# Kernel optimization log

Hardware: AMD Instinct MI355X
Metric: run time of the kernel (lower is better)

The kernel has to match this reference:

```python
import jax, jax.numpy as jnp
import numpy as np

H = 96          # hidden_dim / GatedGraphConv out_channels
L = 6           # num_layers
F_IN = 32       # num_node_features
G = 4096        # number of graphs in batch
BN_EPS = 1e-5


def setup_inputs() -> dict:
    key = jax.random.key(0)
    ks = jax.random.split(key, 16)
    N, E = 100000, 400000
    x = jax.random.normal(ks[0], (N, F_IN), dtype=jnp.float32)
    edge_index = jax.random.randint(ks[1], (2, E), 0, N, dtype=jnp.int64)
    batch = jnp.sort(jax.random.randint(ks[2], (N,), 0, G, dtype=jnp.int64))
    s = 1.0 / np.sqrt(H)
    conv_w = jax.random.uniform(ks[3], (L, H, H), jnp.float32, -s, s)
    w_ih = jax.random.uniform(ks[4], (3 * H, H), jnp.float32, -s, s)
    w_hh = jax.random.uniform(ks[5], (3 * H, H), jnp.float32, -s, s)
    b_ih = jax.random.uniform(ks[6], (3 * H,), jnp.float32, -s, s)
    b_hh = jax.random.uniform(ks[7], (3 * H,), jnp.float32, -s, s)
    bn_gamma = jnp.ones((H,), jnp.float32)
    bn_beta = jnp.zeros((H,), jnp.float32)
    s1 = 1.0 / np.sqrt(H)
    fc1_w = jax.random.uniform(ks[8], (4 * H, H), jnp.float32, -s1, s1)
    fc1_b = jax.random.uniform(ks[9], (4 * H,), jnp.float32, -s1, s1)
    s2 = 1.0 / np.sqrt(4 * H)
    fc2_w = jax.random.uniform(ks[10], (H, 4 * H), jnp.float32, -s2, s2)
    fc2_b = jax.random.uniform(ks[11], (H,), jnp.float32, -s2, s2)
    fc3_w = jax.random.uniform(ks[12], (1, H), jnp.float32, -s1, s1)
    fc3_b = jax.random.uniform(ks[13], (1,), jnp.float32, -s1, s1)
    return dict(x=x, edge_index=edge_index, batch=batch, conv_w=conv_w,
                w_ih=w_ih, w_hh=w_hh, b_ih=b_ih, b_hh=b_hh,
                bn_gamma=bn_gamma, bn_beta=bn_beta,
                fc1_w=fc1_w, fc1_b=fc1_b, fc2_w=fc2_w, fc2_b=fc2_b,
                fc3_w=fc3_w, fc3_b=fc3_b)


def _gated_graph_conv(x, src, dst, conv_w, w_ih, w_hh, b_ih, b_hh):
    N = x.shape[0]
    # PyG zero-pads input features up to out_channels
    h = jnp.pad(x, ((0, 0), (0, H - x.shape[1])))
    for i in range(L):
        m = h @ conv_w[i]                         # [N, H]
        agg = jnp.zeros((N, H), m.dtype).at[dst].add(m[src])  # scatter-add at targets
        gi = agg @ w_ih.T + b_ih                  # [N, 3H]
        gh = h @ w_hh.T + b_hh                    # [N, 3H]
        i_r, i_z, i_n = jnp.split(gi, 3, axis=-1)
        h_r, h_z, h_n = jnp.split(gh, 3, axis=-1)
        r = jax.nn.sigmoid(i_r + h_r)
        z = jax.nn.sigmoid(i_z + h_z)
        n = jnp.tanh(i_n + r * h_n)
        h = (1.0 - z) * n + z * h
    return h


def reference(x, edge_index, batch, conv_w, w_ih, w_hh, b_ih, b_hh,
              bn_gamma, bn_beta, fc1_w, fc1_b, fc2_w, fc2_b, fc3_w, fc3_b):
    src, dst = edge_index[0], edge_index[1]
    h = _gated_graph_conv(x, src, dst, conv_w, w_ih, w_hh, b_ih, b_hh)
    h = jax.nn.relu(h)
    # global mean pool (dropout is identity in eval)
    sums = jax.ops.segment_sum(h, batch, num_segments=G)          # [G, H]
    counts = jax.ops.segment_sum(jnp.ones((h.shape[0],), h.dtype), batch, num_segments=G)
    pooled = sums / jnp.maximum(counts, 1.0)[:, None]
    # BatchNorm1d in eval mode: running_mean=0, running_var=1
    hbn = (pooled / jnp.sqrt(1.0 + BN_EPS)) * bn_gamma + bn_beta
    h1 = jax.nn.relu(hbn @ fc1_w.T + fc1_b)
    h2 = jax.nn.relu(h1 @ fc2_w.T + fc2_b)
    return h2 @ fc3_w.T + fc3_b                                    # [G, 1]
```

## Files before the change

### kernel.cpp

```cpp
#include <hip/hip_runtime.h>

#define H96 96
#define LAYERS 6
#define BN_EPS 1e-5f
#define SCAN_B 1024

typedef unsigned short u16;
typedef unsigned int u32;
typedef _Float16 f16;
typedef _Float16 h8 __attribute__((ext_vector_type(8)));
typedef float f32x4 __attribute__((ext_vector_type(4)));
typedef u32 u32x3 __attribute__((ext_vector_type(3)));

__device__ __forceinline__ float sigm(float x) { return 1.f / (1.f + __expf(-x)); }
__device__ __forceinline__ float tanh_(float x) { return 2.f / (1.f + __expf(-2.f * x)) - 1.f; }
__device__ __forceinline__ f32x4 splat4(float x) { f32x4 v = {x, x, x, x}; return v; }

struct h2s { f16 x, y; };

__device__ __forceinline__ void upk(u32 v, float& lo, float& hi) {
    union { u32 u; h2s h; } c;
    c.u = v;
    lo = (float)c.h.x;
    hi = (float)c.h.y;
}

__global__ void k_f2h(const float* __restrict__ convw, const float* __restrict__ wih,
                      const float* __restrict__ whh, const float* __restrict__ fc1w,
                      const float* __restrict__ fc2w, f16* __restrict__ dst) {
    int i = blockIdx.x * 256 + threadIdx.x;
    if (i >= 184320) return;
    float v;
    if (i < 55296) v = convw[i];
    else if (i < 82944) v = wih[i - 55296];
    else if (i < 110592) v = whh[i - 82944];
    else if (i < 147456) v = fc1w[i - 110592];
    else v = fc2w[i - 147456];
    dst[i] = (f16)v;
}

__global__ __launch_bounds__(256) void k_wpt(const f16* __restrict__ wih16, const f16* __restrict__ convw16,
                                             f16* __restrict__ wpt) {
    int l = blockIdx.y;
    int lane = threadIdx.x & 63, wave = threadIdx.x >> 6;
    int l15 = lane & 15, q = lane >> 4;
    int rowa = blockIdx.x * 64 + wave * 16 + l15;
    if (rowa >= 288) rowa = 287;
    const f16* B = convw16 + (size_t)l * 9216;
    h8 af[3];
#pragma unroll
    for (int s = 0; s < 3; s++) af[s] = *(const h8*)(wih16 + (size_t)rowa * 96 + s * 32 + q * 8);
    f32x4 acc[6];
#pragma unroll
    for (int t = 0; t < 6; t++) acc[t] = splat4(0.f);
#pragma unroll
    for (int s = 0; s < 3; s++)
#pragma unroll
        for (int t = 0; t < 6; t++) {
            h8 b = *(const h8*)(B + (size_t)(t * 16 + l15) * 96 + s * 32 + q * 8);
            acc[t] = __builtin_amdgcn_mfma_f32_16x16x32_f16(af[s], b, acc[t], 0, 0, 0);
        }
    int rbase = blockIdx.x * 64 + wave * 16 + q * 4;
#pragma unroll
    for (int t = 0; t < 6; t++)
#pragma unroll
        for (int rr = 0; rr < 4; rr++) {
            int row = rbase + rr;
            if (row < 288) wpt[(size_t)l * 27648 + (size_t)row * 96 + t * 16 + l15] = (f16)acc[t][rr];
        }
}

__global__ void k_pad(const float* __restrict__ x, f16* __restrict__ hf, int N) {
    int i = blockIdx.x * 256 + threadIdx.x;
    if (i >= N * H96) return;
    int n = i / H96, c = i - n * H96;
    float v = (c < 32) ? x[n * 32 + c] : 0.f;
    hf[i] = (f16)v;
}

__global__ void k_hist(const int* __restrict__ key, int* __restrict__ deg, int E) {
    int e = blockIdx.x * 256 + threadIdx.x;
    if (e < E) atomicAdd(&deg[key[e]], 1);
}

__global__ __launch_bounds__(SCAN_B) void k_scan1(const int* __restrict__ deg, int* __restrict__ incl,
                                                  int* __restrict__ bsum, int N) {
    __shared__ int sh[SCAN_B];
    int i = blockIdx.x * SCAN_B + threadIdx.x;
    int v = (i < N) ? deg[i] : 0;
    sh[threadIdx.x] = v;
    __syncthreads();
    for (int off = 1; off < SCAN_B; off <<= 1) {
        int t = (threadIdx.x >= (u32)off) ? sh[threadIdx.x - off] : 0;
        __syncthreads();
        sh[threadIdx.x] += t;
        __syncthreads();
    }
    incl[blockIdx.x * SCAN_B + threadIdx.x] = sh[threadIdx.x];
    if (threadIdx.x == SCAN_B - 1) bsum[blockIdx.x] = sh[threadIdx.x];
}

__global__ void k_scan2(int* __restrict__ bsum, int nb) {
    if (blockIdx.x == 0 && threadIdx.x == 0) {
        int run = 0;
        for (int i = 0; i < nb; i++) { run += bsum[i]; bsum[i] = run; }
    }
}

__global__ void k_scan3(const int* __restrict__ deg, const int* __restrict__ incl, const int* __restrict__ bsum,
                        int* __restrict__ rs, int* __restrict__ cur, int N, int E) {
    int i = blockIdx.x * 256 + threadIdx.x;
    if (i == 0) rs[N] = E;
    if (i < N) {
        int b = i / SCAN_B;
        int off = (b > 0) ? bsum[b - 1] : 0;
        int ex = incl[i] - deg[i] + off;
        rs[i] = ex;
        if (cur) cur[i] = ex;
    }
}

__global__ void k_fill(const int* __restrict__ src, const int* __restrict__ dst, int* __restrict__ cur,
                       int* __restrict__ es, int E) {
    int e = blockIdx.x * 256 + threadIdx.x;
    if (e < E) {
        int p = atomicAdd(&cur[dst[e]], 1);
        es[p] = src[e];
    }
}

__global__ __launch_bounds__(256) void k_gather(const f16* __restrict__ hin, const int* __restrict__ rs,
                                                const int* __restrict__ es, f16* __restrict__ agg, int N) {
    int grp = threadIdx.x >> 4;
    int lane6 = threadIdx.x & 15;
    int node = blockIdx.x * 16 + grp;
    if (node >= N) return;
    int s = rs[node], e = rs[node + 1];
    float a0 = 0, a1 = 0, a2 = 0, a3 = 0, a4 = 0, a5 = 0;
    const char* basep = (const char*)hin;
    int off = lane6 * 12;
    int i = s;
    for (; i + 4 <= e; i += 4) {
        int sa = es[i], sb = es[i + 1], sc = es[i + 2], sd = es[i + 3];
        u32x3 va = *(const u32x3*)(basep + (size_t)sa * 192 + off);
        u32x3 vb = *(const u32x3*)(basep + (size_t)sb * 192 + off);
        u32x3 vc = *(const u32x3*)(basep + (size_t)sc * 192 + off);
        u32x3 vd = *(const u32x3*)(basep + (size_t)sd * 192 + off);
        float t0, t1;
        upk(va.x, t0, t1); a0 += t0; a1 += t1;
        upk(va.y, t0, t1); a2 += t0; a3 += t1;
        upk(va.z, t0, t1); a4 += t0; a5 += t1;
        upk(vb.x, t0, t1); a0 += t0; a1 += t1;
        upk(vb.y, t0, t1); a2 += t0; a3 += t1;
        upk(vb.z, t0, t1); a4 += t0; a5 += t1;
        upk(vc.x, t0, t1); a0 += t0; a1 += t1;
        upk(vc.y, t0, t1); a2 += t0; a3 += t1;
        upk(vc.z, t0, t1); a4 += t0; a5 += t1;
        upk(vd.x, t0, t1); a0 += t0; a1 += t1;
        upk(vd.y, t0, t1); a2 += t0; a3 += t1;
        upk(vd.z, t0, t1); a4 += t0; a5 += t1;
    }
    for (; i < e; i++) {
        int sa = es[i];
        u32x3 va = *(const u32x3*)(basep + (size_t)sa * 192 + off);
        float t0, t1;
        upk(va.x, t0, t1); a0 += t0; a1 += t1;
        upk(va.y, t0, t1); a2 += t0; a3 += t1;
        upk(va.z, t0, t1); a4 += t0; a5 += t1;
    }
    f16* dp = agg + (size_t)node * H96 + lane6 * 6;
    h2s p0, p1, p2;
    p0.x = (f16)a0; p0.y = (f16)a1;
    p1.x = (f16)a2; p1.y = (f16)a3;
    p2.x = (f16)a4; p2.y = (f16)a5;
    *(h2s*)(dp + 0) = p0;
    *(h2s*)(dp + 2) = p1;
    *(h2s*)(dp + 4) = p2;
}

__global__ __launch_bounds__(384) void k_gru(const f16* __restrict__ agg, const f16* __restrict__ hin,
                                             f16* __restrict__ hout, const f16* __restrict__ wpt,
                                             const f16* __restrict__ whh, const float* __restrict__ bih,
                                             const float* __restrict__ bhh, int N) {
    int w = threadIdx.x >> 6;
    int lane = threadIdx.x & 63;
    int l15 = lane & 15, q = lane >> 4;
    int jr = w * 16 + l15;
    float b_r = bih[jr] + bhh[jr];
    float b_z = bih[96 + jr] + bhh[96 + jr];
    float b_in = bih[192 + jr];
    float b_hn = bhh[192 + jr];
    h8 wr0[3], wr1[3], wz0[3], wz1[3], wn0[3], wn1[3];
#pragma unroll
    for (int s = 0; s < 3; s++) {
        int ko = s * 32 + q * 8;
        wr0[s] = *(const h8*)(wpt + (size_t)jr * H96 + ko);
        wz0[s] = *(const h8*)(wpt + (size_t)(96 + jr) * H96 + ko);
        wn0[s] = *(const h8*)(wpt + (size_t)(192 + jr) * H96 + ko);
        wr1[s] = *(const h8*)(whh + (size_t)jr * H96 + ko);
        wz1[s] = *(const h8*)(whh + (size_t)(96 + jr) * H96 + ko);
        wn1[s] = *(const h8*)(whh + (size_t)(192 + jr) * H96 + ko);
    }
    int ntiles = (N + 15) >> 4;
    for (int tile = blockIdx.x; tile < ntiles; tile += gridDim.x) {
        int base = tile << 4;
        int rowa = base + l15;
        if (rowa >= N) rowa = N - 1;
        h8 as_[3], ah[3];
#pragma unroll
        for (int s = 0; s < 3; s++) {
            as_[s] = *(const h8*)(agg + (size_t)rowa * H96 + s * 32 + q * 8);
            ah[s] = *(const h8*)(hin + (size_t)rowa * H96 + s * 32 + q * 8);
        }
        f32x4 r = splat4(b_r), z = splat4(b_z), nn = splat4(b_in), hn = splat4(b_hn);
#pragma unroll
        for (int s = 0; s < 3; s++) {
            r = __builtin_amdgcn_mfma_f32_16x16x32_f16(as_[s], wr0[s], r, 0, 0, 0);
            r = __builtin_amdgcn_mfma_f32_16x16x32_f16(ah[s], wr1[s], r, 0, 0, 0);
            z = __builtin_amdgcn_mfma_f32_16x16x32_f16(as_[s], wz0[s], z, 0, 0, 0);
            z = __builtin_amdgcn_mfma_f32_16x16x32_f16(ah[s], wz1[s], z, 0, 0, 0);
            nn = __builtin_amdgcn_mfma_f32_16x16x32_f16(as_[s], wn0[s], nn, 0, 0, 0);
            hn = __builtin_amdgcn_mfma_f32_16x16x32_f16(ah[s], wn1[s], hn, 0, 0, 0);
        }
        int rbase = base + q * 4;
#pragma unroll
        for (int rr = 0; rr < 4; rr++) {
            int row = rbase + rr;
            if (row < N) {
                float rv = sigm(r[rr]);
                float zv = sigm(z[rr]);
                float nv = tanh_(nn[rr] + rv * hn[rr]);
                size_t idx = (size_t)row * H96 + w * 16 + l15;
                float hold = (float)hin[idx];
                float hnew = (1.f - zv) * nv + zv * hold;
                hout[idx] = (f16)hnew;
            }
        }
    }
}

__global__ void k_pool2(const f16* __restrict__ hf, const int* __restrict__ grs,
                        const float* __restrict__ gamma, const float* __restrict__ beta,
                        f16* __restrict__ pooled, int Gn) {
    int g = blockIdx.x;
    int c = threadIdx.x;
    if (g >= Gn || c >= H96) return;
    int s = grs[g], e = grs[g + 1];
    float sum = 0.f;
    for (int n = s; n < e; n++) sum += fmaxf((float)hf[(size_t)n * H96 + c], 0.f);
    float cnt = fmaxf((float)(e - s), 1.f);
    float val = (sum / cnt) * (gamma[c] * rsqrtf(1.f + BN_EPS)) + beta[c];
    pooled[(size_t)g * H96 + c] = (f16)val;
}

template <int KS, int NT, bool RELU>
__global__ __launch_bounds__(256) void k_mlp(const f16* __restrict__ A, const f16* __restrict__ W,
                                             const float* __restrict__ bias, f16* __restrict__ out, int M) {
    int lane = threadIdx.x & 63, wave = threadIdx.x >> 6;
    int l15 = lane & 15, q = lane >> 4;
    int tile = blockIdx.x;
    int rowa = tile * 64 + wave * 16 + l15;
    if (rowa >= M) rowa = M - 1;
    h8 af[KS];
#pragma unroll
    for (int s = 0; s < KS; s++) af[s] = *(const h8*)(A + (size_t)rowa * (KS * 32) + s * 32 + q * 8);
    f32x4 acc[NT];
#pragma unroll
    for (int t = 0; t < NT; t++) acc[t] = splat4(0.f);
#pragma unroll
    for (int s = 0; s < KS; s++)
#pragma unroll
        for (int t = 0; t < NT; t++) {
            h8 b = *(const h8*)(W + (size_t)(t * 16 + l15) * (KS * 32) + s * 32 + q * 8);
            acc[t] = __builtin_amdgcn_mfma_f32_16x16x32_f16(af[s], b, acc[t], 0, 0, 0);
        }
    int rbase = tile * 64 + wave * 16 + q * 4;
#pragma unroll
    for (int t = 0; t < NT; t++) {
        float bv = bias[t * 16 + l15];
#pragma unroll
        for (int rr = 0; rr < 4; rr++) {
            int row = rbase + rr;
            if (row >= M) continue;
            float v = acc[t][rr] + bv;
            if (RELU) v = fmaxf(v, 0.f);
            out[(size_t)row * (NT * 16) + t * 16 + l15] = (f16)v;
        }
    }
}

__global__ void k_mlp3(const f16* __restrict__ h2, const float* __restrict__ w, const float* __restrict__ b,
                       float* __restrict__ out, int M) {
    int g = blockIdx.x * 256 + threadIdx.x;
    if (g >= M) return;
    float acc = 0.f;
    for (int k = 0; k < H96; k++) acc += (float)h2[(size_t)g * H96 + k] * w[k];
    out[g] = acc + b[0];
}

extern "C" void kernel_launch(void* const* d_in, const int* in_sizes, int n_in, void* d_out, int out_size,
                              void* d_ws, size_t ws_size, hipStream_t stream) {
    const float* x = (const float*)d_in[0];
    const int* ei = (const int*)d_in[1];
    const int* batch = (const int*)d_in[2];
    const float* conv_w = (const float*)d_in[3];
    const float* wih = (const float*)d_in[4];
    const float* whh = (const float*)d_in[5];
    const float* bih = (const float*)d_in[6];
    const float* bhh = (const float*)d_in[7];
    const float* gamma = (const float*)d_in[8];
    const float* beta = (const float*)d_in[9];
    const float* fc1w = (const float*)d_in[10];
    const float* fc1b = (const float*)d_in[11];
    const float* fc2w = (const float*)d_in[12];
    const float* fc2b = (const float*)d_in[13];
    const float* fc3w = (const float*)d_in[14];
    const float* fc3b = (const float*)d_in[15];

    int N = in_sizes[0] / 32;
    int E = in_sizes[1] / 2;
    int Gn = out_size;
    const int* srcp = ei;
    const int* dstp = ei + E;

    char* p = (char*)d_ws;
    auto alloc = [&](size_t bytes) -> char* {
        char* r = p;
        p += (bytes + 255) & ~(size_t)255;
        return r;
    };
    f16* hA = (f16*)alloc((size_t)N * H96 * 2);
    f16* hB = (f16*)alloc((size_t)N * H96 * 2);
    f16* aggf = (f16*)alloc((size_t)N * H96 * 2);
    f16* wf16 = (f16*)alloc((size_t)184320 * 2);
    f16* wpt = (f16*)alloc((size_t)LAYERS * 27648 * 2);
    int nb = (N + SCAN_B - 1) / SCAN_B;
    int* deg = (int*)alloc((size_t)N * 4);
    int* incl = (int*)alloc((size_t)nb * SCAN_B * 4);
    int* bsum = (int*)alloc((size_t)nb * 4);
    int* rs = (int*)alloc((size_t)(N + 1) * 4);
    int* cur = (int*)alloc((size_t)N * 4);
    int* es = (int*)alloc((size_t)E * 4);
    int nb2 = (Gn + SCAN_B - 1) / SCAN_B;
    int* gdeg = (int*)alloc((size_t)Gn * 4);
    int* gincl = (int*)alloc((size_t)nb2 * SCAN_B * 4);
    int* gbsum = (int*)alloc((size_t)nb2 * 4);
    int* grs = (int*)alloc((size_t)(Gn + 1) * 4);
    f16* pooled = (f16*)alloc((size_t)Gn * H96 * 2);
    f16* h1 = (f16*)alloc((size_t)Gn * 384 * 2);
    f16* h2 = (f16*)alloc((size_t)Gn * H96 * 2);

    f16* convw16 = wf16;
    f16* wih16 = wf16 + 55296;
    f16* whh16 = wf16 + 82944;
    f16* fc1w16 = wf16 + 110592;
    f16* fc2w16 = wf16 + 147456;

    hipMemsetAsync(deg, 0, (size_t)N * 4, stream);
    hipMemsetAsync(gdeg, 0, (size_t)Gn * 4, stream);

    k_f2h<<<720, 256, 0, stream>>>(conv_w, wih, whh, fc1w, fc2w, wf16);
    k_wpt<<<dim3(5, 6), 256, 0, stream>>>(wih16, convw16, wpt);
    k_pad<<<(N * H96 + 255) / 256, 256, 0, stream>>>(x, hA, N);
    k_hist<<<(E + 255) / 256, 256, 0, stream>>>(dstp, deg, E);
    k_scan1<<<nb, SCAN_B, 0, stream>>>(deg, incl, bsum, N);
    k_scan2<<<1, 64, 0, stream>>>(bsum, nb);
    k_scan3<<<(N + 255) / 256, 256, 0, stream>>>(deg, incl, bsum, rs, cur, N, E);
    k_fill<<<(E + 255) / 256, 256, 0, stream>>>(srcp, dstp, cur, es, E);
    k_hist<<<(N + 255) / 256, 256, 0, stream>>>(batch, gdeg, N);
    k_scan1<<<nb2, SCAN_B, 0, stream>>>(gdeg, gincl, gbsum, Gn);
    k_scan2<<<1, 64, 0, stream>>>(gbsum, nb2);
    k_scan3<<<(Gn + 255) / 256, 256, 0, stream>>>(gdeg, gincl, gbsum, grs, (int*)nullptr, Gn, N);

    int nt16 = (N + 15) / 16;
    for (int l = 0; l < LAYERS; l++) {
        f16* hin = (l & 1) ? hB : hA;
        f16* hout = (l & 1) ? hA : hB;
        k_gather<<<nt16, 256, 0, stream>>>(hin, rs, es, aggf, N);
        k_gru<<<1280, 384, 0, stream>>>(aggf, hin, hout, wpt + (size_t)l * 27648, whh16, bih, bhh, N);
    }

    k_pool2<<<Gn, 128, 0, stream>>>(hA, grs, gamma, beta, pooled, Gn);
    k_mlp<3, 24, true><<<(Gn + 63) / 64, 256, 0, stream>>>(pooled, fc1w16, fc1b, h1, Gn);
    k_mlp<12, 6, true><<<(Gn + 63) / 64, 256, 0, stream>>>(h1, fc2w16, fc2b, h2, Gn);
    k_mlp3<<<(Gn + 255) / 256, 256, 0, stream>>>(h2, fc3w, fc3b, (float*)d_out, Gn);
}
```

Measured before the change: 602.8 us.

## Prefetch next GRU tile, mask gather tail, enlarge GRU grid

The GRU kernel now software-pipelines its grid-stride loop: it loads the agg and h rows for the next tile into registers while the MFMAs for the current tile run, so global-load latency overlaps with compute. The gather kernel drops its scalar tail loop and handles the remainder inside the 4-wide loop by clamping indices and multiplying by 0/1 masks. The GRU grid grows from 1280 to 2048 blocks. Extra prefetch registers may lower occupancy, and the masked tail issues redundant loads for nodes whose degree is not a multiple of four.

```diff
diff --git a/kernel.cpp b/kernel.cpp
--- a/kernel.cpp
+++ b/kernel.cpp
@@ -139,9 +139,14 @@
     float a0 = 0, a1 = 0, a2 = 0, a3 = 0, a4 = 0, a5 = 0;
     const char* basep = (const char*)hin;
     int off = lane6 * 12;
-    int i = s;
-    for (; i + 4 <= e; i += 4) {
-        int sa = es[i], sb = es[i + 1], sc = es[i + 2], sd = es[i + 3];
+    for (int i = s; i < e; i += 4) {
+        int j1 = (i + 1 < e) ? i + 1 : i;
+        int j2 = (i + 2 < e) ? i + 2 : i;
+        int j3 = (i + 3 < e) ? i + 3 : i;
+        float m1 = (i + 1 < e) ? 1.f : 0.f;
+        float m2 = (i + 2 < e) ? 1.f : 0.f;
+        float m3 = (i + 3 < e) ? 1.f : 0.f;
+        int sa = es[i], sb = es[j1], sc = es[j2], sd = es[j3];
         u32x3 va = *(const u32x3*)(basep + (size_t)sa * 192 + off);
         u32x3 vb = *(const u32x3*)(basep + (size_t)sb * 192 + off);
         u32x3 vc = *(const u32x3*)(basep + (size_t)sc * 192 + off);
@@ -150,23 +155,15 @@
         upk(va.x, t0, t1); a0 += t0; a1 += t1;
         upk(va.y, t0, t1); a2 += t0; a3 += t1;
         upk(va.z, t0, t1); a4 += t0; a5 += t1;
-        upk(vb.x, t0, t1); a0 += t0; a1 += t1;
-        upk(vb.y, t0, t1); a2 += t0; a3 += t1;
-        upk(vb.z, t0, t1); a4 += t0; a5 += t1;
-        upk(vc.x, t0, t1); a0 += t0; a1 += t1;
-        upk(vc.y, t0, t1); a2 += t0; a3 += t1;
-        upk(vc.z, t0, t1); a4 += t0; a5 += t1;
-        upk(vd.x, t0, t1); a0 += t0; a1 += t1;
-        upk(vd.y, t0, t1); a2 += t0; a3 += t1;
-        upk(vd.z, t0, t1); a4 += t0; a5 += t1;
-    }
-    for (; i < e; i++) {
-        int sa = es[i];
-        u32x3 va = *(const u32x3*)(basep + (size_t)sa * 192 + off);
-        float t0, t1;
-        upk(va.x, t0, t1); a0 += t0; a1 += t1;
-        upk(va.y, t0, t1); a2 += t0; a3 += t1;
-        upk(va.z, t0, t1); a4 += t0; a5 += t1;
+        upk(vb.x, t0, t1); a0 += t0 * m1; a1 += t1 * m1;
+        upk(vb.y, t0, t1); a2 += t0 * m1; a3 += t1 * m1;
+        upk(vb.z, t0, t1); a4 += t0 * m1; a5 += t1 * m1;
+        upk(vc.x, t0, t1); a0 += t0 * m2; a1 += t1 * m2;
+        upk(vc.y, t0, t1); a2 += t0 * m2; a3 += t1 * m2;
+        upk(vc.z, t0, t1); a4 += t0 * m2; a5 += t1 * m2;
+        upk(vd.x, t0, t1); a0 += t0 * m3; a1 += t1 * m3;
+        upk(vd.y, t0, t1); a2 += t0 * m3; a3 += t1 * m3;
+        upk(vd.z, t0, t1); a4 += t0 * m3; a5 += t1 * m3;
     }
     f16* dp = agg + (size_t)node * H96 + lane6 * 6;
     h2s p0, p1, p2;
@@ -202,26 +199,42 @@
         wn1[s] = *(const h8*)(whh + (size_t)(192 + jr) * H96 + ko);
     }
     int ntiles = (N + 15) >> 4;
-    for (int tile = blockIdx.x; tile < ntiles; tile += gridDim.x) {
+    int tile = blockIdx.x;
+    if (tile >= ntiles) return;
+    int ko = (q >> 0) * 8;
+    h8 as0[3], ah0[3];
+    {
+        int rowa = (tile << 4) + l15;
+        if (rowa >= N) rowa = N - 1;
+#pragma unroll
+        for (int s = 0; s < 3; s++) {
+            as0[s] = *(const h8*)(agg + (size_t)rowa * H96 + s * 32 + q * 8);
+            ah0[s] = *(const h8*)(hin + (size_t)rowa * H96 + s * 32 + q * 8);
+        }
+    }
+    for (; tile < ntiles; tile += gridDim.x) {
+        int nxt = tile + gridDim.x;
+        h8 as1[3], ah1[3];
+        if (nxt < ntiles) {
+            int rowa = (nxt << 4) + l15;
+            if (rowa >= N) rowa = N - 1;
+#pragma unroll
+            for (int s = 0; s < 3; s++) {
+                as1[s] = *(const h8*)(agg + (size_t)rowa * H96 + s * 32 + q * 8);
+                ah1[s] = *(const h8*)(hin + (size_t)rowa * H96 + s * 32 + q * 8);
+            }
+        }
+        f32x4 r = splat4(b_r), z = splat4(b_z), nn = splat4(b_in), hn = splat4(b_hn);
+#pragma unroll
+        for (int s = 0; s < 3; s++) {
+            r = __builtin_amdgcn_mfma_f32_16x16x32_f16(as0[s], wr0[s], r, 0, 0, 0);
+            r = __builtin_amdgcn_mfma_f32_16x16x32_f16(ah0[s], wr1[s], r, 0, 0, 0);
+            z = __builtin_amdgcn_mfma_f32_16x16x32_f16(as0[s], wz0[s], z, 0, 0, 0);
+            z = __builtin_amdgcn_mfma_f32_16x16x32_f16(ah0[s], wz1[s], z, 0, 0, 0);
+            nn = __builtin_amdgcn_mfma_f32_16x16x32_f16(as0[s], wn0[s], nn, 0, 0, 0);
+            hn = __builtin_amdgcn_mfma_f32_16x16x32_f16(ah0[s], wn1[s], hn, 0, 0, 0);
+        }
         int base = tile << 4;
-        int rowa = base + l15;
-        if (rowa >= N) rowa = N - 1;
-        h8 as_[3], ah[3];
-#pragma unroll
-        for (int s = 0; s < 3; s++) {
-            as_[s] = *(const h8*)(agg + (size_t)rowa * H96 + s * 32 + q * 8);
-            ah[s] = *(const h8*)(hin + (size_t)rowa * H96 + s * 32 + q * 8);
-        }
-        f32x4 r = splat4(b_r), z = splat4(b_z), nn = splat4(b_in), hn = splat4(b_hn);
-#pragma unroll
-        for (int s = 0; s < 3; s++) {
-            r = __builtin_amdgcn_mfma_f32_16x16x32_f16(as_[s], wr0[s], r, 0, 0, 0);
-            r = __builtin_amdgcn_mfma_f32_16x16x32_f16(ah[s], wr1[s], r, 0, 0, 0);
-            z = __builtin_amdgcn_mfma_f32_16x16x32_f16(as_[s], wz0[s], z, 0, 0, 0);
-            z = __builtin_amdgcn_mfma_f32_16x16x32_f16(ah[s], wz1[s], z, 0, 0, 0);
-            nn = __builtin_amdgcn_mfma_f32_16x16x32_f16(as_[s], wn0[s], nn, 0, 0, 0);
-            hn = __builtin_amdgcn_mfma_f32_16x16x32_f16(ah[s], wn1[s], hn, 0, 0, 0);
-        }
         int rbase = base + q * 4;
 #pragma unroll
         for (int rr = 0; rr < 4; rr++) {
@@ -236,7 +249,13 @@
                 hout[idx] = (f16)hnew;
             }
         }
-    }
+#pragma unroll
+        for (int s = 0; s < 3; s++) {
+            as0[s] = as1[s];
+            ah0[s] = ah1[s];
+        }
+    }
+    (void)ko;
 }
 
 __global__ void k_pool2(const f16* __restrict__ hf, const int* __restrict__ grs,
@@ -377,7 +396,7 @@
         f16* hin = (l & 1) ? hB : hA;
         f16* hout = (l & 1) ? hA : hB;
         k_gather<<<nt16, 256, 0, stream>>>(hin, rs, es, aggf, N);
-        k_gru<<<1280, 384, 0, stream>>>(aggf, hin, hout, wpt + (size_t)l * 27648, whh16, bih, bhh, N);
+        k_gru<<<2048, 384, 0, stream>>>(aggf, hin, hout, wpt + (size_t)l * 27648, whh16, bih, bhh, N);
     }
 
     k_pool2<<<Gn, 128, 0, stream>>>(hA, grs, gamma, beta, pooled, Gn);
```

Measured after the change: 654.3 us. 1.09x slower.

## Mask gather tail, set GRU occupancy bound, split fc1 across column blocks

Applied to the files above, without the earlier changes.

The gather loop now always processes edges in groups of four. Out-of-range slots reuse the first index and are zeroed by a multiplicative mask, which replaces the scalar remainder loop. The GRU kernel gets a minimum-blocks-per-SM launch bound of 4, limiting registers per thread to raise occupancy. The fc1 MLP is split over a second grid dimension of four column blocks, giving more parallel blocks and fewer accumulators per thread. The costs are redundant masked loads and FMAs in the gather, and possible register spills in the GRU.

```diff
diff --git a/kernel.cpp b/kernel.cpp
--- a/kernel.cpp
+++ b/kernel.cpp
@@ -139,9 +139,14 @@
     float a0 = 0, a1 = 0, a2 = 0, a3 = 0, a4 = 0, a5 = 0;
     const char* basep = (const char*)hin;
     int off = lane6 * 12;
-    int i = s;
-    for (; i + 4 <= e; i += 4) {
-        int sa = es[i], sb = es[i + 1], sc = es[i + 2], sd = es[i + 3];
+    for (int i = s; i < e; i += 4) {
+        int j1 = (i + 1 < e) ? i + 1 : i;
+        int j2 = (i + 2 < e) ? i + 2 : i;
+        int j3 = (i + 3 < e) ? i + 3 : i;
+        float m1 = (i + 1 < e) ? 1.f : 0.f;
+        float m2 = (i + 2 < e) ? 1.f : 0.f;
+        float m3 = (i + 3 < e) ? 1.f : 0.f;
+        int sa = es[i], sb = es[j1], sc = es[j2], sd = es[j3];
         u32x3 va = *(const u32x3*)(basep + (size_t)sa * 192 + off);
         u32x3 vb = *(const u32x3*)(basep + (size_t)sb * 192 + off);
         u32x3 vc = *(const u32x3*)(basep + (size_t)sc * 192 + off);
@@ -150,23 +155,15 @@
         upk(va.x, t0, t1); a0 += t0; a1 += t1;
         upk(va.y, t0, t1); a2 += t0; a3 += t1;
         upk(va.z, t0, t1); a4 += t0; a5 += t1;
-        upk(vb.x, t0, t1); a0 += t0; a1 += t1;
-        upk(vb.y, t0, t1); a2 += t0; a3 += t1;
-        upk(vb.z, t0, t1); a4 += t0; a5 += t1;
-        upk(vc.x, t0, t1); a0 += t0; a1 += t1;
-        upk(vc.y, t0, t1); a2 += t0; a3 += t1;
-        upk(vc.z, t0, t1); a4 += t0; a5 += t1;
-        upk(vd.x, t0, t1); a0 += t0; a1 += t1;
-        upk(vd.y, t0, t1); a2 += t0; a3 += t1;
-        upk(vd.z, t0, t1); a4 += t0; a5 += t1;
-    }
-    for (; i < e; i++) {
-        int sa = es[i];
-        u32x3 va = *(const u32x3*)(basep + (size_t)sa * 192 + off);
-        float t0, t1;
-        upk(va.x, t0, t1); a0 += t0; a1 += t1;
-        upk(va.y, t0, t1); a2 += t0; a3 += t1;
-        upk(va.z, t0, t1); a4 += t0; a5 += t1;
+        upk(vb.x, t0, t1); a0 += t0 * m1; a1 += t1 * m1;
+        upk(vb.y, t0, t1); a2 += t0 * m1; a3 += t1 * m1;
+        upk(vb.z, t0, t1); a4 += t0 * m1; a5 += t1 * m1;
+        upk(vc.x, t0, t1); a0 += t0 * m2; a1 += t1 * m2;
+        upk(vc.y, t0, t1); a2 += t0 * m2; a3 += t1 * m2;
+        upk(vc.z, t0, t1); a4 += t0 * m2; a5 += t1 * m2;
+        upk(vd.x, t0, t1); a0 += t0 * m3; a1 += t1 * m3;
+        upk(vd.y, t0, t1); a2 += t0 * m3; a3 += t1 * m3;
+        upk(vd.z, t0, t1); a4 += t0 * m3; a5 += t1 * m3;
     }
     f16* dp = agg + (size_t)node * H96 + lane6 * 6;
     h2s p0, p1, p2;
@@ -178,10 +175,10 @@
     *(h2s*)(dp + 4) = p2;
 }
 
-__global__ __launch_bounds__(384) void k_gru(const f16* __restrict__ agg, const f16* __restrict__ hin,
-                                             f16* __restrict__ hout, const f16* __restrict__ wpt,
-                                             const f16* __restrict__ whh, const float* __restrict__ bih,
-                                             const float* __restrict__ bhh, int N) {
+__global__ __launch_bounds__(384, 4) void k_gru(const f16* __restrict__ agg, const f16* __restrict__ hin,
+                                                f16* __restrict__ hout, const f16* __restrict__ wpt,
+                                                const f16* __restrict__ whh, const float* __restrict__ bih,
+                                                const float* __restrict__ bhh, int N) {
     int w = threadIdx.x >> 6;
     int lane = threadIdx.x & 63;
     int l15 = lane & 15, q = lane >> 4;
@@ -253,11 +250,12 @@
     pooled[(size_t)g * H96 + c] = (f16)val;
 }
 
-template <int KS, int NT, bool RELU>
+template <int KS, int NT, int OUTW, bool RELU>
 __global__ __launch_bounds__(256) void k_mlp(const f16* __restrict__ A, const f16* __restrict__ W,
                                              const float* __restrict__ bias, f16* __restrict__ out, int M) {
     int lane = threadIdx.x & 63, wave = threadIdx.x >> 6;
     int l15 = lane & 15, q = lane >> 4;
+    int colBase = blockIdx.y * (NT * 16);
     int tile = blockIdx.x;
     int rowa = tile * 64 + wave * 16 + l15;
     if (rowa >= M) rowa = M - 1;
@@ -271,20 +269,20 @@
     for (int s = 0; s < KS; s++)
 #pragma unroll
         for (int t = 0; t < NT; t++) {
-            h8 b = *(const h8*)(W + (size_t)(t * 16 + l15) * (KS * 32) + s * 32 + q * 8);
+            h8 b = *(const h8*)(W + (size_t)(colBase + t * 16 + l15) * (KS * 32) + s * 32 + q * 8);
             acc[t] = __builtin_amdgcn_mfma_f32_16x16x32_f16(af[s], b, acc[t], 0, 0, 0);
         }
     int rbase = tile * 64 + wave * 16 + q * 4;
 #pragma unroll
     for (int t = 0; t < NT; t++) {
-        float bv = bias[t * 16 + l15];
+        float bv = bias[colBase + t * 16 + l15];
 #pragma unroll
         for (int rr = 0; rr < 4; rr++) {
             int row = rbase + rr;
             if (row >= M) continue;
             float v = acc[t][rr] + bv;
             if (RELU) v = fmaxf(v, 0.f);
-            out[(size_t)row * (NT * 16) + t * 16 + l15] = (f16)v;
+            out[(size_t)row * OUTW + colBase + t * 16 + l15] = (f16)v;
         }
     }
 }
@@ -381,7 +379,7 @@
     }
 
     k_pool2<<<Gn, 128, 0, stream>>>(hA, grs, gamma, beta, pooled, Gn);
-    k_mlp<3, 24, true><<<(Gn + 63) / 64, 256, 0, stream>>>(pooled, fc1w16, fc1b, h1, Gn);
-    k_mlp<12, 6, true><<<(Gn + 63) / 64, 256, 0, stream>>>(h1, fc2w16, fc2b, h2, Gn);
+    k_mlp<3, 6, 384, true><<<dim3((Gn + 63) / 64, 4), 256, 0, stream>>>(pooled, fc1w16, fc1b, h1, Gn);
+    k_mlp<12, 6, 96, true><<<dim3((Gn + 63) / 64, 1), 256, 0, stream>>>(h1, fc2w16, fc2b, h2, Gn);
     k_mlp3<<<(Gn + 255) / 256, 256, 0, stream>>>(h2, fc3w, fc3b, (float*)d_out, Gn);
 }
```

After: 558.1 us. 1.08x faster.
